# Kernel optimization log

Measured on AMD Instinct MI355X. Metric: run time of the kernel, lower is better.

The kernel has to match this reference:

```python
import jax, jax.numpy as jnp
import numpy as np

B, C_IN, C_OUT, N, E = 1, 64, 64, 100000, 3200000
BN_EPS = 1e-5


def setup_inputs() -> dict:
    key = jax.random.key(0)
    ks = jax.random.split(key, 8)
    return {
        "in_features": jax.random.normal(ks[0], (B, C_IN, N), dtype=jnp.float32),
        "w_v": jax.random.normal(ks[1], (C_OUT, C_IN), dtype=jnp.float32) * (1.0 / np.sqrt(C_IN)),
        "w_n": jax.random.normal(ks[2], (C_OUT, C_IN), dtype=jnp.float32) * (1.0 / np.sqrt(C_IN)),
        "gamma": jnp.ones((C_OUT,), dtype=jnp.float32),
        "beta": jnp.zeros((C_OUT,), dtype=jnp.float32),
        "prelu_a": jnp.full((1,), 0.25, dtype=jnp.float32),
        "reduce_index": jax.random.randint(ks[3], (E,), 0, N, dtype=jnp.int32),
        "gather_index": jax.random.randint(ks[4], (E,), 0, N, dtype=jnp.int32),
    }


def reference(in_features, w_v, w_n, gamma, beta, prelu_a, reduce_index, gather_index):
    # 1x1 convs == per-node linear maps: [B, C_in, N] -> [B, C_out, N]
    F_v = jnp.einsum('oi,bin->bon', w_v, in_features)
    F_n = jnp.einsum('oi,bin->bon', w_n, in_features)

    # gather source-node features per edge: [E, B, C_out]
    src = jnp.moveaxis(F_n[:, :, gather_index], 2, 0)
    # scatter-mean into destination nodes (include_self=False -> 0 for isolated nodes)
    sums = jax.ops.segment_sum(src, reduce_index, num_segments=N)  # [N, B, C]
    counts = jax.ops.segment_sum(jnp.ones((src.shape[0],), src.dtype), reduce_index,
                                 num_segments=N)  # [N]
    mean = sums / jnp.maximum(counts, 1.0)[:, None, None]  # nodes w/o edges stay 0
    out = jnp.moveaxis(mean, 0, 2) + F_v  # [B, C, N]

    # BatchNorm1d (training mode: biased batch stats over (B, N))
    mu = jnp.mean(out, axis=(0, 2), keepdims=True)
    var = jnp.mean((out - mu) ** 2, axis=(0, 2), keepdims=True)
    out = (out - mu) * jax.lax.rsqrt(var + BN_EPS)
    out = out * gamma[None, :, None] + beta[None, :, None]

    # PReLU with a single shared learnable slope
    out = jnp.where(out >= 0, out, prelu_a[0] * out)
    return out
```

## Files before the change

kernel.cpp:

```cpp
#include <hip/hip_runtime.h>
#include <hip/hip_bf16.h>

#define NODES 100000
#define BN_EPS 1e-5f
#define NB2 256
#define NPB2 391
#define CAP 13072
#define EPB 2048

__device__ __forceinline__ unsigned bf16rne(float f) {
    unsigned u = __float_as_uint(f);
    u += 0x7FFFu + ((u >> 16) & 1u);
    return u >> 16;
}
__device__ __forceinline__ float bflo(unsigned u) { return __uint_as_float(u << 16); }
__device__ __forceinline__ float bfhi(unsigned u) { return __uint_as_float(u & 0xFFFF0000u); }

__global__ __launch_bounds__(256, 8) void k_place(
        const int* __restrict__ ridx, const int* __restrict__ gidx,
        int* __restrict__ cursor, unsigned* __restrict__ packed, int E) {
    __shared__ int lh[4][NB2];
    const int t = threadIdx.x;
    const int w = t >> 6;
    for (int k = t; k < 4 * NB2; k += 256) ((int*)lh)[k] = 0;
    __syncthreads();
    const int base = blockIdx.x * EPB;
    int r[EPB / 256], g[EPB / 256];
#pragma unroll
    for (int k = 0; k < EPB / 256; ++k) {
        int e = base + t + (k << 8);
        r[k] = (e < E) ? ridx[e] : -1;
        g[k] = (e < E) ? gidx[e] : 0;
    }
#pragma unroll
    for (int k = 0; k < EPB / 256; ++k)
        if (r[k] >= 0) atomicAdd(&lh[w][(unsigned)r[k] / NPB2], 1);
    __syncthreads();
    {
        int c0 = lh[0][t], c1 = lh[1][t], c2 = lh[2][t], c3 = lh[3][t];
        int tot = c0 + c1 + c2 + c3;
        if (tot) {
            int g0 = t * CAP + atomicAdd(&cursor[t], tot);
            lh[0][t] = g0;
            lh[1][t] = g0 + c0;
            lh[2][t] = g0 + c0 + c1;
            lh[3][t] = g0 + c0 + c1 + c2;
        }
    }
    __syncthreads();
#pragma unroll
    for (int k = 0; k < EPB / 256; ++k) {
        if (r[k] >= 0) {
            unsigned rr = (unsigned)r[k];
            unsigned b = rr / NPB2;
            int off = atomicAdd(&lh[w][b], 1);
            if (off < (int)((b + 1) * CAP))
                packed[off] = ((rr - b * NPB2) << 17) | (unsigned)g[k];
        }
    }
}

__global__ __launch_bounds__(1024) void k_sortb(
        const int* __restrict__ cursor, unsigned* __restrict__ packed,
        int* __restrict__ nodestart, int* __restrict__ cnt) {
    __shared__ int lh[1024];
    __shared__ int lsc[1024];
    const int b = blockIdx.x, t = threadIdx.x;
    const int s0b = b * CAP;
    int cntb = cursor[b];
    if (cntb > CAP) cntb = CAP;
    unsigned r[(CAP + 1023) / 1024];
#pragma unroll
    for (int kk = 0; kk < (CAP + 1023) / 1024; ++kk) {
        int k = t + kk * 1024;
        if (k < cntb) r[kk] = packed[s0b + k];
    }
    lh[t] = 0;
    __syncthreads();
#pragma unroll
    for (int kk = 0; kk < (CAP + 1023) / 1024; ++kk) {
        int k = t + kk * 1024;
        if (k < cntb) atomicAdd(&lh[r[kk] >> 17], 1);
    }
    __syncthreads();
    lsc[t] = lh[t];
    __syncthreads();
    for (int off = 1; off < 1024; off <<= 1) {
        int v = lsc[t];
        int add = (t >= off) ? lsc[t - off] : 0;
        __syncthreads();
        lsc[t] = v + add;
        __syncthreads();
    }
    int excl = (t == 0) ? 0 : lsc[t - 1];
    if (t < NPB2) {
        int n = b * NPB2 + t;
        if (n < NODES) {
            nodestart[n] = s0b + excl;
            cnt[n] = lh[t];
        }
    }
    __syncthreads();
    lh[t] = excl;
    __syncthreads();
#pragma unroll
    for (int kk = 0; kk < (CAP + 1023) / 1024; ++kk) {
        int k = t + kk * 1024;
        if (k < cntb) {
            unsigned v = r[kk];
            int pos = atomicAdd(&lh[v >> 17], 1);
            packed[s0b + pos] = v & 0x1FFFFu;
        }
    }
}

__global__ __launch_bounds__(256, 4) void k_gemm_bf16(
        const float* __restrict__ x, const float* __restrict__ wn,
        unsigned* __restrict__ Fnh2) {
    __shared__ float lx[64 * 68];
    __shared__ float wt[64 * 68];
    const int t = threadIdx.x;
    const int n0 = blockIdx.x * 64;
    for (int idx = t; idx < 1024; idx += 256) {
        int rr = idx >> 4;
        int q4 = (idx & 15) * 4;
        int n = n0 + q4;
        float4 xv = {0.f, 0.f, 0.f, 0.f};
        if (n < NODES) xv = *(const float4*)(x + rr * NODES + n);
        *(float4*)&lx[rr * 68 + q4] = xv;
        float4 w4 = *(const float4*)(wn + (idx << 2));
        wt[(q4 + 0) * 68 + rr] = w4.x;
        wt[(q4 + 1) * 68 + rr] = w4.y;
        wt[(q4 + 2) * 68 + rr] = w4.z;
        wt[(q4 + 3) * 68 + rr] = w4.w;
    }
    __syncthreads();
    const int c4 = (t & 15) * 4;
    const int j4 = (t >> 4) * 4;
    float4 a0 = {0,0,0,0}, a1 = {0,0,0,0}, a2 = {0,0,0,0}, a3 = {0,0,0,0};
#pragma unroll 8
    for (int ci = 0; ci < 64; ++ci) {
        float4 w = *(const float4*)&wt[ci * 68 + c4];
        float4 xv = *(const float4*)&lx[ci * 68 + j4];
        a0.x += w.x * xv.x; a0.y += w.x * xv.y; a0.z += w.x * xv.z; a0.w += w.x * xv.w;
        a1.x += w.y * xv.x; a1.y += w.y * xv.y; a1.z += w.y * xv.z; a1.w += w.y * xv.w;
        a2.x += w.z * xv.x; a2.y += w.z * xv.y; a2.z += w.z * xv.z; a2.w += w.z * xv.w;
        a3.x += w.w * xv.x; a3.y += w.w * xv.y; a3.z += w.w * xv.z; a3.w += w.w * xv.w;
    }
    uint2* F2 = (uint2*)Fnh2;
#pragma unroll
    for (int k = 0; k < 4; ++k) {
        int n = n0 + j4 + k;
        if (n < NODES) {
            float v0 = (k == 0) ? a0.x : (k == 1) ? a0.y : (k == 2) ? a0.z : a0.w;
            float v1 = (k == 0) ? a1.x : (k == 1) ? a1.y : (k == 2) ? a1.z : a1.w;
            float v2 = (k == 0) ? a2.x : (k == 1) ? a2.y : (k == 2) ? a2.z : a2.w;
            float v3 = (k == 0) ? a3.x : (k == 1) ? a3.y : (k == 2) ? a3.z : a3.w;
            uint2 val;
            val.x = bf16rne(v0) | (bf16rne(v1) << 16);
            val.y = bf16rne(v2) | (bf16rne(v3) << 16);
            F2[n * 16 + (c4 >> 2)] = val;
        }
    }
}

__global__ __launch_bounds__(256) void k_gemm_n(
        const float* __restrict__ x, const float* __restrict__ wn,
        float* __restrict__ Fn) {
    __shared__ float lx[64][65];
    __shared__ float lw[64][65];
    const int t = threadIdx.x;
    const int n0 = blockIdx.x * 64;
    for (int idx = t; idx < 4096; idx += 256) {
        int r = idx >> 6, q = idx & 63;
        lw[r][q] = wn[idx];
        int n = n0 + q;
        lx[r][q] = (n < NODES) ? x[r * NODES + n] : 0.f;
    }
    __syncthreads();
    const int c = t & 63;
    const int jb = t >> 6;
    for (int k = 0; k < 16; ++k) {
        int j = jb + 4 * k;
        int n = n0 + j;
        if (n >= NODES) continue;
        float acc = 0.f;
#pragma unroll
        for (int ci = 0; ci < 64; ++ci)
            acc += lw[c][ci] * lx[ci][j];
        Fn[n * 64 + c] = acc;
    }
}

__global__ __launch_bounds__(256) void k_segreduce(
        const unsigned* __restrict__ Fnh2, const unsigned* __restrict__ packed,
        const int* __restrict__ nodestart, const int* __restrict__ cnt,
        float4* __restrict__ mean4) {
    const int n = (int)((blockIdx.x * 256u + threadIdx.x) >> 6);
    if (n >= NODES) return;
    const int lane = threadIdx.x & 63;
    const int sub = lane >> 3;
    const int cp  = lane & 7;
    const int s0 = nodestart[n];
    const int cn = cnt[n];
    const int s1 = s0 + cn;
    float f0 = 0.f, f1 = 0.f, f2 = 0.f, f3 = 0.f;
    float f4 = 0.f, f5 = 0.f, f6 = 0.f, f7 = 0.f;
    int i = s0;
    for (; i + 15 < s1; i += 16) {
        int ga = (int)packed[i + sub];
        int gb = (int)packed[i + 8 + sub];
        uint4 ua = *(const uint4*)(Fnh2 + (((size_t)ga) << 5) + (cp << 2));
        uint4 ub = *(const uint4*)(Fnh2 + (((size_t)gb) << 5) + (cp << 2));
        f0 += bflo(ua.x) + bflo(ub.x);
        f1 += bfhi(ua.x) + bfhi(ub.x);
        f2 += bflo(ua.y) + bflo(ub.y);
        f3 += bfhi(ua.y) + bfhi(ub.y);
        f4 += bflo(ua.z) + bflo(ub.z);
        f5 += bfhi(ua.z) + bfhi(ub.z);
        f6 += bflo(ua.w) + bflo(ub.w);
        f7 += bfhi(ua.w) + bfhi(ub.w);
    }
    for (; i < s1; i += 8) {
        uint4 u = {0u, 0u, 0u, 0u};
        if (i + sub < s1) {
            int g = (int)packed[i + sub];
            u = *(const uint4*)(Fnh2 + (((size_t)g) << 5) + (cp << 2));
        }
        f0 += bflo(u.x); f1 += bfhi(u.x);
        f2 += bflo(u.y); f3 += bfhi(u.y);
        f4 += bflo(u.z); f5 += bfhi(u.z);
        f6 += bflo(u.w); f7 += bfhi(u.w);
    }
#pragma unroll
    for (int m = 8; m < 64; m <<= 1) {
        f0 += __shfl_xor(f0, m);
        f1 += __shfl_xor(f1, m);
        f2 += __shfl_xor(f2, m);
        f3 += __shfl_xor(f3, m);
        f4 += __shfl_xor(f4, m);
        f5 += __shfl_xor(f5, m);
        f6 += __shfl_xor(f6, m);
        f7 += __shfl_xor(f7, m);
    }
    if (sub == 0) {
        float inv = 1.f / fmaxf((float)cn, 1.f);
        float4 lo4, hi4;
        lo4.x = f0 * inv; lo4.y = f1 * inv; lo4.z = f2 * inv; lo4.w = f3 * inv;
        hi4.x = f4 * inv; hi4.y = f5 * inv; hi4.z = f6 * inv; hi4.w = f7 * inv;
        mean4[n * 16 + cp * 2]     = lo4;
        mean4[n * 16 + cp * 2 + 1] = hi4;
    }
}

__global__ __launch_bounds__(256, 4) void k_combine(
        const float* __restrict__ x, const float* __restrict__ wv,
        const float* __restrict__ sums, const int* __restrict__ counts,
        const int divide,
        float* __restrict__ outpre, float* __restrict__ bn) {
    __shared__ float lx[64 * 68];
    __shared__ float wt[64 * 68];
    __shared__ float reds[64][5];
    __shared__ float redq[64][5];
    const int t = threadIdx.x;
    const int n0 = blockIdx.x * 64;
    const int c4 = (t & 15) * 4;
    const int j4 = (t >> 4) * 4;
    float4 mv[4];
    const float4* sums4 = (const float4*)sums;
#pragma unroll
    for (int k = 0; k < 4; ++k) {
        int n = n0 + j4 + k;
        mv[k] = (n < NODES) ? sums4[n * 16 + (c4 >> 2)]
                            : float4{0.f, 0.f, 0.f, 0.f};
    }
    for (int idx = t; idx < 1024; idx += 256) {
        int rr = idx >> 4;
        int q4 = (idx & 15) * 4;
        int n = n0 + q4;
        float4 xv = {0.f, 0.f, 0.f, 0.f};
        if (n < NODES) xv = *(const float4*)(x + rr * NODES + n);
        *(float4*)&lx[rr * 68 + q4] = xv;
        float4 w4 = *(const float4*)(wv + (idx << 2));
        wt[(q4 + 0) * 68 + rr] = w4.x;
        wt[(q4 + 1) * 68 + rr] = w4.y;
        wt[(q4 + 2) * 68 + rr] = w4.z;
        wt[(q4 + 3) * 68 + rr] = w4.w;
    }
    __syncthreads();
    float4 a0 = {0,0,0,0}, a1 = {0,0,0,0}, a2 = {0,0,0,0}, a3 = {0,0,0,0};
#pragma unroll 8
    for (int ci = 0; ci < 64; ++ci) {
        float4 w = *(const float4*)&wt[ci * 68 + c4];
        float4 xv = *(const float4*)&lx[ci * 68 + j4];
        a0.x += w.x * xv.x; a0.y += w.x * xv.y; a0.z += w.x * xv.z; a0.w += w.x * xv.w;
        a1.x += w.y * xv.x; a1.y += w.y * xv.y; a1.z += w.y * xv.z; a1.w += w.y * xv.w;
        a2.x += w.z * xv.x; a2.y += w.z * xv.y; a2.z += w.z * xv.z; a2.w += w.z * xv.w;
        a3.x += w.w * xv.x; a3.y += w.w * xv.y; a3.z += w.w * xv.z; a3.w += w.w * xv.w;
    }
    __syncthreads();
    float* tile = wt;
    float ls0 = 0.f, ls1 = 0.f, ls2 = 0.f, ls3 = 0.f;
    float lq0 = 0.f, lq1 = 0.f, lq2 = 0.f, lq3 = 0.f;
#pragma unroll
    for (int k = 0; k < 4; ++k) {
        int j = j4 + k;
        int n = n0 + j;
        float v0 = 0.f, v1 = 0.f, v2 = 0.f, v3 = 0.f;
        if (n < NODES) {
            float4 m = mv[k];
            if (divide) {
                float cf = fmaxf((float)counts[n], 1.f);
                m.x /= cf; m.y /= cf; m.z /= cf; m.w /= cf;
            }
            float b0 = (k == 0) ? a0.x : (k == 1) ? a0.y : (k == 2) ? a0.z : a0.w;
            float b1 = (k == 0) ? a1.x : (k == 1) ? a1.y : (k == 2) ? a1.z : a1.w;
            float b2 = (k == 0) ? a2.x : (k == 1) ? a2.y : (k == 2) ? a2.z : a2.w;
            float b3 = (k == 0) ? a3.x : (k == 1) ? a3.y : (k == 2) ? a3.z : a3.w;
            v0 = m.x + b0; v1 = m.y + b1; v2 = m.z + b2; v3 = m.w + b3;
            ls0 += v0; lq0 += v0 * v0;
            ls1 += v1; lq1 += v1 * v1;
            ls2 += v2; lq2 += v2 * v2;
            ls3 += v3; lq3 += v3 * v3;
        }
        tile[(c4 + 0) * 65 + j] = v0;
        tile[(c4 + 1) * 65 + j] = v1;
        tile[(c4 + 2) * 65 + j] = v2;
        tile[(c4 + 3) * 65 + j] = v3;
    }
    const int lane = t & 63;
    const int wid = t >> 6;
#pragma unroll
    for (int m = 16; m < 64; m <<= 1) {
        ls0 += __shfl_xor(ls0, m); lq0 += __shfl_xor(lq0, m);
        ls1 += __shfl_xor(ls1, m); lq1 += __shfl_xor(lq1, m);
        ls2 += __shfl_xor(ls2, m); lq2 += __shfl_xor(lq2, m);
        ls3 += __shfl_xor(ls3, m); lq3 += __shfl_xor(lq3, m);
    }
    if (lane < 16) {
        reds[lane * 4 + 0][wid] = ls0; redq[lane * 4 + 0][wid] = lq0;
        reds[lane * 4 + 1][wid] = ls1; redq[lane * 4 + 1][wid] = lq1;
        reds[lane * 4 + 2][wid] = ls2; redq[lane * 4 + 2][wid] = lq2;
        reds[lane * 4 + 3][wid] = ls3; redq[lane * 4 + 3][wid] = lq3;
    }
    __syncthreads();
    const int j2 = t & 63;
    const int c2 = t >> 6;
    const int n = n0 + j2;
    if (n < NODES) {
        for (int k = 0; k < 16; ++k) {
            int cc = c2 + 4 * k;
            outpre[cc * NODES + n] = tile[cc * 65 + j2];
        }
    }
    if (t < 64) {
        float s = reds[t][0] + reds[t][1] + reds[t][2] + reds[t][3];
        float q = redq[t][0] + redq[t][1] + redq[t][2] + redq[t][3];
        atomicAdd(&bn[t], s);
        atomicAdd(&bn[64 + t], q);
    }
}

__global__ __launch_bounds__(256) void k_final(
        float* __restrict__ out, const float* __restrict__ bn,
        const float* __restrict__ gamma, const float* __restrict__ beta,
        const float* __restrict__ pa) {
    const int c = blockIdx.y;
    const int n = blockIdx.x * 256 + threadIdx.x;
    const float invN = 1.f / (float)NODES;
    float mu = bn[c] * invN;
    float var = fmaxf(bn[64 + c] * invN - mu * mu, 0.f);
    float scale = gamma[c] * rsqrtf(var + BN_EPS);
    float shift = beta[c] - mu * scale;
    float a = pa[0];
    if (n < NODES) {
        float y = out[c * NODES + n] * scale + shift;
        y = (y >= 0.f) ? y : a * y;
        out[c * NODES + n] = y;
    }
}

__global__ __launch_bounds__(256) void k_scatter(
        const float* __restrict__ Fn,
        const int* __restrict__ gidx, const int* __restrict__ ridx,
        float* __restrict__ sums, int* __restrict__ counts, int E) {
    const int wave = (int)((blockIdx.x * blockDim.x + threadIdx.x) >> 6);
    const int lane = threadIdx.x & 63;
    const int base = wave * 64;
    if (base >= E) return;
    const int nvalid = min(64, E - base);
    int g = 0, r = 0;
    if (lane < nvalid) {
        g = gidx[base + lane];
        r = ridx[base + lane];
        atomicAdd(&counts[r], 1);
    }
    for (int i = 0; i < nvalid; ++i) {
        int gg = __shfl(g, i);
        int rr = __shfl(r, i);
        float v = Fn[gg * 64 + lane];
        atomicAdd(&sums[rr * 64 + lane], v);
    }
}

extern "C" void kernel_launch(void* const* d_in, const int* in_sizes, int n_in,
                              void* d_out, int out_size, void* d_ws, size_t ws_size,
                              hipStream_t stream) {
    const float* x     = (const float*)d_in[0];
    const float* w_v   = (const float*)d_in[1];
    const float* w_n   = (const float*)d_in[2];
    const float* gamma = (const float*)d_in[3];
    const float* beta  = (const float*)d_in[4];
    const float* pa    = (const float*)d_in[5];
    const int* ridx    = (const int*)d_in[6];
    const int* gidx    = (const int*)d_in[7];
    float* out = (float*)d_out;

    const int E = in_sizes[6];
    const long long N64 = (long long)NODES * 64;
    const int ntiles = (NODES + 63) / 64;
    const dim3 g4((NODES + 255) / 256, 64);

    size_t need = ((size_t)N64 + (size_t)NB2 * CAP + NB2 + 128
                   + NODES + NODES) * 4;

    if (ws_size >= need) {
        float*    mean      = (float*)d_ws;
        unsigned* packed    = (unsigned*)(mean + N64);
        int*      cursor    = (int*)(packed + (size_t)NB2 * CAP);
        float*    bn        = (float*)(cursor + NB2);
        int*      nodestart = (int*)(bn + 128);
        int*      cntarr    = nodestart + NODES;
        unsigned* Fnh2 = (unsigned*)out;

        hipMemsetAsync(cursor, 0, (NB2 + 128) * sizeof(int), stream);
        k_place<<<(E + EPB - 1) / EPB, 256, 0, stream>>>(ridx, gidx, cursor,
                                                         packed, E);
        k_gemm_bf16<<<ntiles, 256, 0, stream>>>(x, w_n, Fnh2);
        k_sortb<<<NB2, 1024, 0, stream>>>(cursor, packed, nodestart, cntarr);
        k_segreduce<<<(NODES * 64 + 255) / 256, 256, 0, stream>>>(
            Fnh2, packed, nodestart, cntarr, (float4*)mean);
        k_combine<<<ntiles, 256, 0, stream>>>(x, w_v, mean, cntarr, 0, out, bn);
        k_final<<<g4, 256, 0, stream>>>(out, bn, gamma, beta, pa);
    } else {
        float* sums   = (float*)d_ws;
        int*   counts = (int*)(sums + N64);
        float* bn     = (float*)(sums + N64 + NODES);
        float* Fn = out;

        hipMemsetAsync(sums, 0, (size_t)(N64 + NODES + 128) * sizeof(float),
                       stream);
        k_gemm_n<<<ntiles, 256, 0, stream>>>(x, w_n, Fn);
        k_scatter<<<(E + 255) / 256, 256, 0, stream>>>(Fn, gidx, ridx, sums,
                                                       counts, E);
        k_combine<<<ntiles, 256, 0, stream>>>(x, w_v, sums, counts, 1, out, bn);
        k_final<<<g4, 256, 0, stream>>>(out, bn, gamma, beta, pa);
    }
}
```

Measured before the change: 293.6 us.

## Split bf16 gathered features into channel planes and reduce per plane

The GEMM now writes F_n in bf16 as four planes of 16 channels each (32 bytes per node per plane) instead of one interleaved 128-byte row. The segment reduce runs four times, once per plane, so each pass touches a 3.2 MB working set that fits better in cache for the random gathers. The edge index loads use nontemporal hints. In exchange, the packed indices and node starts are re-read four times and there are four launches instead of one.

```diff
diff --git a/kernel.cpp b/kernel.cpp
--- a/kernel.cpp
+++ b/kernel.cpp
@@ -148,6 +148,8 @@
         a3.x += w.w * xv.x; a3.y += w.w * xv.y; a3.z += w.w * xv.z; a3.w += w.w * xv.w;
     }
     uint2* F2 = (uint2*)Fnh2;
+    const int kb = c4 >> 4;
+    const int d2 = (c4 & 15) >> 2;
 #pragma unroll
     for (int k = 0; k < 4; ++k) {
         int n = n0 + j4 + k;
@@ -159,7 +161,7 @@
             uint2 val;
             val.x = bf16rne(v0) | (bf16rne(v1) << 16);
             val.y = bf16rne(v2) | (bf16rne(v3) << 16);
-            F2[n * 16 + (c4 >> 2)] = val;
+            F2[(size_t)kb * (NODES * 4) + n * 4 + d2] = val;
         }
     }
 }
@@ -192,64 +194,51 @@
     }
 }
 
-__global__ __launch_bounds__(256) void k_segreduce(
-        const unsigned* __restrict__ Fnh2, const unsigned* __restrict__ packed,
+__global__ __launch_bounds__(256) void k_segreduce_p(
+        const unsigned* __restrict__ plane, const unsigned* __restrict__ packed,
         const int* __restrict__ nodestart, const int* __restrict__ cnt,
-        float4* __restrict__ mean4) {
+        float4* __restrict__ mean4, const int kb4) {
     const int n = (int)((blockIdx.x * 256u + threadIdx.x) >> 6);
     if (n >= NODES) return;
     const int lane = threadIdx.x & 63;
-    const int sub = lane >> 3;
-    const int cp  = lane & 7;
+    const int sub = lane >> 2;
+    const int cp  = lane & 3;
     const int s0 = nodestart[n];
     const int cn = cnt[n];
     const int s1 = s0 + cn;
     float f0 = 0.f, f1 = 0.f, f2 = 0.f, f3 = 0.f;
-    float f4 = 0.f, f5 = 0.f, f6 = 0.f, f7 = 0.f;
     int i = s0;
-    for (; i + 15 < s1; i += 16) {
-        int ga = (int)packed[i + sub];
-        int gb = (int)packed[i + 8 + sub];
-        uint4 ua = *(const uint4*)(Fnh2 + (((size_t)ga) << 5) + (cp << 2));
-        uint4 ub = *(const uint4*)(Fnh2 + (((size_t)gb) << 5) + (cp << 2));
+    for (; i + 31 < s1; i += 32) {
+        int ga = (int)__builtin_nontemporal_load(&packed[i + sub]);
+        int gb = (int)__builtin_nontemporal_load(&packed[i + 16 + sub]);
+        uint2 ua = *(const uint2*)(plane + (((size_t)ga) << 3) + (cp << 1));
+        uint2 ub = *(const uint2*)(plane + (((size_t)gb) << 3) + (cp << 1));
         f0 += bflo(ua.x) + bflo(ub.x);
         f1 += bfhi(ua.x) + bfhi(ub.x);
         f2 += bflo(ua.y) + bflo(ub.y);
         f3 += bfhi(ua.y) + bfhi(ub.y);
-        f4 += bflo(ua.z) + bflo(ub.z);
-        f5 += bfhi(ua.z) + bfhi(ub.z);
-        f6 += bflo(ua.w) + bflo(ub.w);
-        f7 += bfhi(ua.w) + bfhi(ub.w);
-    }
-    for (; i < s1; i += 8) {
-        uint4 u = {0u, 0u, 0u, 0u};
+    }
+    for (; i < s1; i += 16) {
+        uint2 u = {0u, 0u};
         if (i + sub < s1) {
             int g = (int)packed[i + sub];
-            u = *(const uint4*)(Fnh2 + (((size_t)g) << 5) + (cp << 2));
+            u = *(const uint2*)(plane + (((size_t)g) << 3) + (cp << 1));
         }
         f0 += bflo(u.x); f1 += bfhi(u.x);
         f2 += bflo(u.y); f3 += bfhi(u.y);
-        f4 += bflo(u.z); f5 += bfhi(u.z);
-        f6 += bflo(u.w); f7 += bfhi(u.w);
-    }
-#pragma unroll
-    for (int m = 8; m < 64; m <<= 1) {
+    }
+#pragma unroll
+    for (int m = 4; m < 64; m <<= 1) {
         f0 += __shfl_xor(f0, m);
         f1 += __shfl_xor(f1, m);
         f2 += __shfl_xor(f2, m);
         f3 += __shfl_xor(f3, m);
-        f4 += __shfl_xor(f4, m);
-        f5 += __shfl_xor(f5, m);
-        f6 += __shfl_xor(f6, m);
-        f7 += __shfl_xor(f7, m);
     }
     if (sub == 0) {
         float inv = 1.f / fmaxf((float)cn, 1.f);
-        float4 lo4, hi4;
-        lo4.x = f0 * inv; lo4.y = f1 * inv; lo4.z = f2 * inv; lo4.w = f3 * inv;
-        hi4.x = f4 * inv; hi4.y = f5 * inv; hi4.z = f6 * inv; hi4.w = f7 * inv;
-        mean4[n * 16 + cp * 2]     = lo4;
-        mean4[n * 16 + cp * 2 + 1] = hi4;
+        float4 v;
+        v.x = f0 * inv; v.y = f1 * inv; v.z = f2 * inv; v.w = f3 * inv;
+        mean4[n * 16 + kb4 + cp] = v;
     }
 }
 
@@ -438,8 +427,11 @@
                                                          packed, E);
         k_gemm_bf16<<<ntiles, 256, 0, stream>>>(x, w_n, Fnh2);
         k_sortb<<<NB2, 1024, 0, stream>>>(cursor, packed, nodestart, cntarr);
-        k_segreduce<<<(NODES * 64 + 255) / 256, 256, 0, stream>>>(
-            Fnh2, packed, nodestart, cntarr, (float4*)mean);
+        for (int kb = 0; kb < 4; ++kb) {
+            k_segreduce_p<<<(NODES * 64 + 255) / 256, 256, 0, stream>>>(
+                Fnh2 + (size_t)kb * NODES * 8, packed, nodestart, cntarr,
+                (float4*)mean, kb * 4);
+        }
         k_combine<<<ntiles, 256, 0, stream>>>(x, w_v, mean, cntarr, 0, out, bn);
         k_final<<<g4, 256, 0, stream>>>(out, bn, gamma, beta, pa);
     } else {
```

After: 397.0 us. 1.35x slower.

## Stream x directly from global in combine and store float4 outputs without LDS tile

Applied to the files above, without the earlier changes.

The combine kernel no longer stages the input feature tile in shared memory. Each thread now reads float4 slices of x straight from global memory inside the channel loop, and writes its 4x4 output block as float4 stores directly to outpre instead of transposing through an LDS tile. This drops one LDS buffer and one barrier and raises the occupancy hint from 4 to 8 blocks. The trade-off is that x is re-read by the 16 channel-group threads per node group, relying on cache hits, and the output stores are 16-byte strided writes rather than coalesced row writes.

```diff
diff --git a/kernel.cpp b/kernel.cpp
--- a/kernel.cpp
+++ b/kernel.cpp
@@ -253,81 +253,78 @@
     }
 }
 
-__global__ __launch_bounds__(256, 4) void k_combine(
+__global__ __launch_bounds__(256, 8) void k_combine(
         const float* __restrict__ x, const float* __restrict__ wv,
         const float* __restrict__ sums, const int* __restrict__ counts,
         const int divide,
         float* __restrict__ outpre, float* __restrict__ bn) {
-    __shared__ float lx[64 * 68];
     __shared__ float wt[64 * 68];
     __shared__ float reds[64][5];
     __shared__ float redq[64][5];
     const int t = threadIdx.x;
     const int n0 = blockIdx.x * 64;
-    const int c4 = (t & 15) * 4;
-    const int j4 = (t >> 4) * 4;
-    float4 mv[4];
-    const float4* sums4 = (const float4*)sums;
-#pragma unroll
-    for (int k = 0; k < 4; ++k) {
-        int n = n0 + j4 + k;
-        mv[k] = (n < NODES) ? sums4[n * 16 + (c4 >> 2)]
-                            : float4{0.f, 0.f, 0.f, 0.f};
-    }
     for (int idx = t; idx < 1024; idx += 256) {
-        int rr = idx >> 4;
-        int q4 = (idx & 15) * 4;
-        int n = n0 + q4;
-        float4 xv = {0.f, 0.f, 0.f, 0.f};
-        if (n < NODES) xv = *(const float4*)(x + rr * NODES + n);
-        *(float4*)&lx[rr * 68 + q4] = xv;
-        float4 w4 = *(const float4*)(wv + (idx << 2));
+        int rr = idx & 63;
+        int q4 = (idx >> 6) * 4;
+        float4 w4 = *(const float4*)(wv + rr * 64 + q4);
         wt[(q4 + 0) * 68 + rr] = w4.x;
         wt[(q4 + 1) * 68 + rr] = w4.y;
         wt[(q4 + 2) * 68 + rr] = w4.z;
         wt[(q4 + 3) * 68 + rr] = w4.w;
     }
     __syncthreads();
+    const int c4 = (t & 15) * 4;
+    const int j4 = (t >> 4) * 4;
+    const int jn = n0 + j4;
+    const bool valid = (jn < NODES);
+    const int jc = valid ? jn : 0;
     float4 a0 = {0,0,0,0}, a1 = {0,0,0,0}, a2 = {0,0,0,0}, a3 = {0,0,0,0};
-#pragma unroll 8
+#pragma unroll 4
     for (int ci = 0; ci < 64; ++ci) {
         float4 w = *(const float4*)&wt[ci * 68 + c4];
-        float4 xv = *(const float4*)&lx[ci * 68 + j4];
+        float4 xv = *(const float4*)(x + (size_t)ci * NODES + jc);
         a0.x += w.x * xv.x; a0.y += w.x * xv.y; a0.z += w.x * xv.z; a0.w += w.x * xv.w;
         a1.x += w.y * xv.x; a1.y += w.y * xv.y; a1.z += w.y * xv.z; a1.w += w.y * xv.w;
         a2.x += w.z * xv.x; a2.y += w.z * xv.y; a2.z += w.z * xv.z; a2.w += w.z * xv.w;
         a3.x += w.w * xv.x; a3.y += w.w * xv.y; a3.z += w.w * xv.z; a3.w += w.w * xv.w;
     }
-    __syncthreads();
-    float* tile = wt;
-    float ls0 = 0.f, ls1 = 0.f, ls2 = 0.f, ls3 = 0.f;
-    float lq0 = 0.f, lq1 = 0.f, lq2 = 0.f, lq3 = 0.f;
-#pragma unroll
-    for (int k = 0; k < 4; ++k) {
-        int j = j4 + k;
-        int n = n0 + j;
-        float v0 = 0.f, v1 = 0.f, v2 = 0.f, v3 = 0.f;
-        if (n < NODES) {
-            float4 m = mv[k];
-            if (divide) {
-                float cf = fmaxf((float)counts[n], 1.f);
-                m.x /= cf; m.y /= cf; m.z /= cf; m.w /= cf;
-            }
-            float b0 = (k == 0) ? a0.x : (k == 1) ? a0.y : (k == 2) ? a0.z : a0.w;
-            float b1 = (k == 0) ? a1.x : (k == 1) ? a1.y : (k == 2) ? a1.z : a1.w;
-            float b2 = (k == 0) ? a2.x : (k == 1) ? a2.y : (k == 2) ? a2.z : a2.w;
-            float b3 = (k == 0) ? a3.x : (k == 1) ? a3.y : (k == 2) ? a3.z : a3.w;
-            v0 = m.x + b0; v1 = m.y + b1; v2 = m.z + b2; v3 = m.w + b3;
-            ls0 += v0; lq0 += v0 * v0;
-            ls1 += v1; lq1 += v1 * v1;
-            ls2 += v2; lq2 += v2 * v2;
-            ls3 += v3; lq3 += v3 * v3;
-        }
-        tile[(c4 + 0) * 65 + j] = v0;
-        tile[(c4 + 1) * 65 + j] = v1;
-        tile[(c4 + 2) * 65 + j] = v2;
-        tile[(c4 + 3) * 65 + j] = v3;
-    }
+    const float4* sums4 = (const float4*)sums;
+    float4 mv0 = {0,0,0,0}, mv1 = {0,0,0,0}, mv2 = {0,0,0,0}, mv3 = {0,0,0,0};
+    if (valid) {
+        mv0 = sums4[(jn + 0) * 16 + (c4 >> 2)];
+        mv1 = sums4[(jn + 1) * 16 + (c4 >> 2)];
+        mv2 = sums4[(jn + 2) * 16 + (c4 >> 2)];
+        mv3 = sums4[(jn + 3) * 16 + (c4 >> 2)];
+        if (divide) {
+            float i0 = 1.f / fmaxf((float)counts[jn + 0], 1.f);
+            float i1 = 1.f / fmaxf((float)counts[jn + 1], 1.f);
+            float i2 = 1.f / fmaxf((float)counts[jn + 2], 1.f);
+            float i3 = 1.f / fmaxf((float)counts[jn + 3], 1.f);
+            mv0.x *= i0; mv0.y *= i0; mv0.z *= i0; mv0.w *= i0;
+            mv1.x *= i1; mv1.y *= i1; mv1.z *= i1; mv1.w *= i1;
+            mv2.x *= i2; mv2.y *= i2; mv2.z *= i2; mv2.w *= i2;
+            mv3.x *= i3; mv3.y *= i3; mv3.z *= i3; mv3.w *= i3;
+        }
+    }
+    float4 st0 = {0,0,0,0}, st1 = {0,0,0,0}, st2 = {0,0,0,0}, st3 = {0,0,0,0};
+    if (valid) {
+        st0.x = mv0.x + a0.x; st0.y = mv1.x + a0.y; st0.z = mv2.x + a0.z; st0.w = mv3.x + a0.w;
+        st1.x = mv0.y + a1.x; st1.y = mv1.y + a1.y; st1.z = mv2.y + a1.z; st1.w = mv3.y + a1.w;
+        st2.x = mv0.z + a2.x; st2.y = mv1.z + a2.y; st2.z = mv2.z + a2.z; st2.w = mv3.z + a2.w;
+        st3.x = mv0.w + a3.x; st3.y = mv1.w + a3.y; st3.z = mv2.w + a3.z; st3.w = mv3.w + a3.w;
+        *(float4*)(outpre + (size_t)(c4 + 0) * NODES + jn) = st0;
+        *(float4*)(outpre + (size_t)(c4 + 1) * NODES + jn) = st1;
+        *(float4*)(outpre + (size_t)(c4 + 2) * NODES + jn) = st2;
+        *(float4*)(outpre + (size_t)(c4 + 3) * NODES + jn) = st3;
+    }
+    float ls0 = st0.x + st0.y + st0.z + st0.w;
+    float ls1 = st1.x + st1.y + st1.z + st1.w;
+    float ls2 = st2.x + st2.y + st2.z + st2.w;
+    float ls3 = st3.x + st3.y + st3.z + st3.w;
+    float lq0 = st0.x*st0.x + st0.y*st0.y + st0.z*st0.z + st0.w*st0.w;
+    float lq1 = st1.x*st1.x + st1.y*st1.y + st1.z*st1.z + st1.w*st1.w;
+    float lq2 = st2.x*st2.x + st2.y*st2.y + st2.z*st2.z + st2.w*st2.w;
+    float lq3 = st3.x*st3.x + st3.y*st3.y + st3.z*st3.z + st3.w*st3.w;
     const int lane = t & 63;
     const int wid = t >> 6;
 #pragma unroll
@@ -344,15 +341,6 @@
         reds[lane * 4 + 3][wid] = ls3; redq[lane * 4 + 3][wid] = lq3;
     }
     __syncthreads();
-    const int j2 = t & 63;
-    const int c2 = t >> 6;
-    const int n = n0 + j2;
-    if (n < NODES) {
-        for (int k = 0; k < 16; ++k) {
-            int cc = c2 + 4 * k;
-            outpre[cc * NODES + n] = tile[cc * 65 + j2];
-        }
-    }
     if (t < 64) {
         float s = reds[t][0] + reds[t][1] + reds[t][2] + reds[t][3];
         float q = redq[t][0] + redq[t][1] + redq[t][2] + redq[t][3];
```

Result: slower. 300.5 us (+2.4%).

## Aggregate raw inputs before applying neighbor weight matrix, fuse both GEMMs in combine

Applied to the files above, without the earlier changes.

Exploits linearity of the neighbor 1x1 conv: the edge mean is computed over bf16-transposed input features, and W_n is applied afterwards inside the combine kernel alongside W_v. The standalone neighbor GEMM kernel becomes a plain transpose/convert kernel. This removes a separate GEMM pass and its compute in exchange for an extra in-tile GEMM and transposed staging of the mean in the combine kernel; bf16 rounding now applies to inputs rather than projected features.

```diff
diff --git a/kernel.cpp b/kernel.cpp
--- a/kernel.cpp
+++ b/kernel.cpp
@@ -114,11 +114,9 @@
     }
 }
 
-__global__ __launch_bounds__(256, 4) void k_gemm_bf16(
-        const float* __restrict__ x, const float* __restrict__ wn,
-        unsigned* __restrict__ Fnh2) {
+__global__ __launch_bounds__(256, 4) void k_xpose(
+        const float* __restrict__ x, unsigned* __restrict__ xb2) {
     __shared__ float lx[64 * 68];
-    __shared__ float wt[64 * 68];
     const int t = threadIdx.x;
     const int n0 = blockIdx.x * 64;
     for (int idx = t; idx < 1024; idx += 256) {
@@ -126,36 +124,21 @@
         int q4 = (idx & 15) * 4;
         int n = n0 + q4;
         float4 xv = {0.f, 0.f, 0.f, 0.f};
-        if (n < NODES) xv = *(const float4*)(x + rr * NODES + n);
+        if (n < NODES) xv = *(const float4*)(x + (size_t)rr * NODES + n);
         *(float4*)&lx[rr * 68 + q4] = xv;
-        float4 w4 = *(const float4*)(wn + (idx << 2));
-        wt[(q4 + 0) * 68 + rr] = w4.x;
-        wt[(q4 + 1) * 68 + rr] = w4.y;
-        wt[(q4 + 2) * 68 + rr] = w4.z;
-        wt[(q4 + 3) * 68 + rr] = w4.w;
     }
     __syncthreads();
     const int c4 = (t & 15) * 4;
     const int j4 = (t >> 4) * 4;
-    float4 a0 = {0,0,0,0}, a1 = {0,0,0,0}, a2 = {0,0,0,0}, a3 = {0,0,0,0};
-#pragma unroll 8
-    for (int ci = 0; ci < 64; ++ci) {
-        float4 w = *(const float4*)&wt[ci * 68 + c4];
-        float4 xv = *(const float4*)&lx[ci * 68 + j4];
-        a0.x += w.x * xv.x; a0.y += w.x * xv.y; a0.z += w.x * xv.z; a0.w += w.x * xv.w;
-        a1.x += w.y * xv.x; a1.y += w.y * xv.y; a1.z += w.y * xv.z; a1.w += w.y * xv.w;
-        a2.x += w.z * xv.x; a2.y += w.z * xv.y; a2.z += w.z * xv.z; a2.w += w.z * xv.w;
-        a3.x += w.w * xv.x; a3.y += w.w * xv.y; a3.z += w.w * xv.z; a3.w += w.w * xv.w;
-    }
-    uint2* F2 = (uint2*)Fnh2;
+    uint2* F2 = (uint2*)xb2;
 #pragma unroll
     for (int k = 0; k < 4; ++k) {
         int n = n0 + j4 + k;
         if (n < NODES) {
-            float v0 = (k == 0) ? a0.x : (k == 1) ? a0.y : (k == 2) ? a0.z : a0.w;
-            float v1 = (k == 0) ? a1.x : (k == 1) ? a1.y : (k == 2) ? a1.z : a1.w;
-            float v2 = (k == 0) ? a2.x : (k == 1) ? a2.y : (k == 2) ? a2.z : a2.w;
-            float v3 = (k == 0) ? a3.x : (k == 1) ? a3.y : (k == 2) ? a3.z : a3.w;
+            float v0 = lx[(c4 + 0) * 68 + j4 + k];
+            float v1 = lx[(c4 + 1) * 68 + j4 + k];
+            float v2 = lx[(c4 + 2) * 68 + j4 + k];
+            float v3 = lx[(c4 + 3) * 68 + j4 + k];
             uint2 val;
             val.x = bf16rne(v0) | (bf16rne(v1) << 16);
             val.y = bf16rne(v2) | (bf16rne(v3) << 16);
@@ -253,7 +236,129 @@
     }
 }
 
-__global__ __launch_bounds__(256, 4) void k_combine(
+__global__ __launch_bounds__(256, 4) void k_combine128(
+        const float* __restrict__ x, const float* __restrict__ wv,
+        const float* __restrict__ wn, const float* __restrict__ meanx,
+        float* __restrict__ outpre, float* __restrict__ bn) {
+    __shared__ float lx[64 * 68];
+    __shared__ float wt[64 * 68];
+    __shared__ float reds[64][5];
+    __shared__ float redq[64][5];
+    const int t = threadIdx.x;
+    const int n0 = blockIdx.x * 64;
+    const int c4 = (t & 15) * 4;
+    const int j4 = (t >> 4) * 4;
+    for (int idx = t; idx < 1024; idx += 256) {
+        int rr = idx >> 4;
+        int q4 = (idx & 15) * 4;
+        int n = n0 + q4;
+        float4 xv = {0.f, 0.f, 0.f, 0.f};
+        if (n < NODES) xv = *(const float4*)(x + (size_t)rr * NODES + n);
+        *(float4*)&lx[rr * 68 + q4] = xv;
+        float4 w4 = *(const float4*)(wv + (idx << 2));
+        wt[(q4 + 0) * 68 + rr] = w4.x;
+        wt[(q4 + 1) * 68 + rr] = w4.y;
+        wt[(q4 + 2) * 68 + rr] = w4.z;
+        wt[(q4 + 3) * 68 + rr] = w4.w;
+    }
+    __syncthreads();
+    float4 a0 = {0,0,0,0}, a1 = {0,0,0,0}, a2 = {0,0,0,0}, a3 = {0,0,0,0};
+#pragma unroll 8
+    for (int ci = 0; ci < 64; ++ci) {
+        float4 w = *(const float4*)&wt[ci * 68 + c4];
+        float4 xv = *(const float4*)&lx[ci * 68 + j4];
+        a0.x += w.x * xv.x; a0.y += w.x * xv.y; a0.z += w.x * xv.z; a0.w += w.x * xv.w;
+        a1.x += w.y * xv.x; a1.y += w.y * xv.y; a1.z += w.y * xv.z; a1.w += w.y * xv.w;
+        a2.x += w.z * xv.x; a2.y += w.z * xv.y; a2.z += w.z * xv.z; a2.w += w.z * xv.w;
+        a3.x += w.w * xv.x; a3.y += w.w * xv.y; a3.z += w.w * xv.z; a3.w += w.w * xv.w;
+    }
+    __syncthreads();
+    for (int idx = t; idx < 1024; idx += 256) {
+        int j  = idx >> 4;
+        int ci4 = (idx & 15) * 4;
+        int n = n0 + j;
+        float4 m4 = {0.f, 0.f, 0.f, 0.f};
+        if (n < NODES) m4 = *(const float4*)(meanx + (size_t)n * 64 + ci4);
+        lx[(ci4 + 0) * 68 + j] = m4.x;
+        lx[(ci4 + 1) * 68 + j] = m4.y;
+        lx[(ci4 + 2) * 68 + j] = m4.z;
+        lx[(ci4 + 3) * 68 + j] = m4.w;
+        int rr = idx >> 4;
+        int q4 = (idx & 15) * 4;
+        float4 w4 = *(const float4*)(wn + (idx << 2));
+        wt[(q4 + 0) * 68 + rr] = w4.x;
+        wt[(q4 + 1) * 68 + rr] = w4.y;
+        wt[(q4 + 2) * 68 + rr] = w4.z;
+        wt[(q4 + 3) * 68 + rr] = w4.w;
+    }
+    __syncthreads();
+#pragma unroll 8
+    for (int ci = 0; ci < 64; ++ci) {
+        float4 w = *(const float4*)&wt[ci * 68 + c4];
+        float4 xv = *(const float4*)&lx[ci * 68 + j4];
+        a0.x += w.x * xv.x; a0.y += w.x * xv.y; a0.z += w.x * xv.z; a0.w += w.x * xv.w;
+        a1.x += w.y * xv.x; a1.y += w.y * xv.y; a1.z += w.y * xv.z; a1.w += w.y * xv.w;
+        a2.x += w.z * xv.x; a2.y += w.z * xv.y; a2.z += w.z * xv.z; a2.w += w.z * xv.w;
+        a3.x += w.w * xv.x; a3.y += w.w * xv.y; a3.z += w.w * xv.z; a3.w += w.w * xv.w;
+    }
+    __syncthreads();
+    float* tile = wt;
+    float ls0 = 0.f, ls1 = 0.f, ls2 = 0.f, ls3 = 0.f;
+    float lq0 = 0.f, lq1 = 0.f, lq2 = 0.f, lq3 = 0.f;
+#pragma unroll
+    for (int k = 0; k < 4; ++k) {
+        int j = j4 + k;
+        int n = n0 + j;
+        float v0 = 0.f, v1 = 0.f, v2 = 0.f, v3 = 0.f;
+        if (n < NODES) {
+            v0 = (k == 0) ? a0.x : (k == 1) ? a0.y : (k == 2) ? a0.z : a0.w;
+            v1 = (k == 0) ? a1.x : (k == 1) ? a1.y : (k == 2) ? a1.z : a1.w;
+            v2 = (k == 0) ? a2.x : (k == 1) ? a2.y : (k == 2) ? a2.z : a2.w;
+            v3 = (k == 0) ? a3.x : (k == 1) ? a3.y : (k == 2) ? a3.z : a3.w;
+            ls0 += v0; lq0 += v0 * v0;
+            ls1 += v1; lq1 += v1 * v1;
+            ls2 += v2; lq2 += v2 * v2;
+            ls3 += v3; lq3 += v3 * v3;
+        }
+        tile[(c4 + 0) * 65 + j] = v0;
+        tile[(c4 + 1) * 65 + j] = v1;
+        tile[(c4 + 2) * 65 + j] = v2;
+        tile[(c4 + 3) * 65 + j] = v3;
+    }
+    const int lane = t & 63;
+    const int wid = t >> 6;
+#pragma unroll
+    for (int m = 16; m < 64; m <<= 1) {
+        ls0 += __shfl_xor(ls0, m); lq0 += __shfl_xor(lq0, m);
+        ls1 += __shfl_xor(ls1, m); lq1 += __shfl_xor(lq1, m);
+        ls2 += __shfl_xor(ls2, m); lq2 += __shfl_xor(lq2, m);
+        ls3 += __shfl_xor(ls3, m); lq3 += __shfl_xor(lq3, m);
+    }
+    if (lane < 16) {
+        reds[lane * 4 + 0][wid] = ls0; redq[lane * 4 + 0][wid] = lq0;
+        reds[lane * 4 + 1][wid] = ls1; redq[lane * 4 + 1][wid] = lq1;
+        reds[lane * 4 + 2][wid] = ls2; redq[lane * 4 + 2][wid] = lq2;
+        reds[lane * 4 + 3][wid] = ls3; redq[lane * 4 + 3][wid] = lq3;
+    }
+    __syncthreads();
+    const int j2 = t & 63;
+    const int c2 = t >> 6;
+    const int n = n0 + j2;
+    if (n < NODES) {
+        for (int k = 0; k < 16; ++k) {
+            int cc = c2 + 4 * k;
+            outpre[cc * NODES + n] = tile[cc * 65 + j2];
+        }
+    }
+    if (t < 64) {
+        float s = reds[t][0] + reds[t][1] + reds[t][2] + reds[t][3];
+        float q = redq[t][0] + redq[t][1] + redq[t][2] + redq[t][3];
+        atomicAdd(&bn[t], s);
+        atomicAdd(&bn[64 + t], q);
+    }
+}
+
+__global__ __launch_bounds__(256, 4) void k_combine_fb(
         const float* __restrict__ x, const float* __restrict__ wv,
         const float* __restrict__ sums, const int* __restrict__ counts,
         const int divide,
@@ -279,7 +384,7 @@
         int q4 = (idx & 15) * 4;
         int n = n0 + q4;
         float4 xv = {0.f, 0.f, 0.f, 0.f};
-        if (n < NODES) xv = *(const float4*)(x + rr * NODES + n);
+        if (n < NODES) xv = *(const float4*)(x + (size_t)rr * NODES + n);
         *(float4*)&lx[rr * 68 + q4] = xv;
         float4 w4 = *(const float4*)(wv + (idx << 2));
         wt[(q4 + 0) * 68 + rr] = w4.x;
@@ -425,22 +530,22 @@
                    + NODES + NODES) * 4;
 
     if (ws_size >= need) {
-        float*    mean      = (float*)d_ws;
-        unsigned* packed    = (unsigned*)(mean + N64);
+        float*    meanx     = (float*)d_ws;
+        unsigned* packed    = (unsigned*)(meanx + N64);
         int*      cursor    = (int*)(packed + (size_t)NB2 * CAP);
         float*    bn        = (float*)(cursor + NB2);
         int*      nodestart = (int*)(bn + 128);
         int*      cntarr    = nodestart + NODES;
-        unsigned* Fnh2 = (unsigned*)out;
+        unsigned* xb = (unsigned*)out;
 
         hipMemsetAsync(cursor, 0, (NB2 + 128) * sizeof(int), stream);
         k_place<<<(E + EPB - 1) / EPB, 256, 0, stream>>>(ridx, gidx, cursor,
                                                          packed, E);
-        k_gemm_bf16<<<ntiles, 256, 0, stream>>>(x, w_n, Fnh2);
+        k_xpose<<<ntiles, 256, 0, stream>>>(x, xb);
         k_sortb<<<NB2, 1024, 0, stream>>>(cursor, packed, nodestart, cntarr);
         k_segreduce<<<(NODES * 64 + 255) / 256, 256, 0, stream>>>(
-            Fnh2, packed, nodestart, cntarr, (float4*)mean);
-        k_combine<<<ntiles, 256, 0, stream>>>(x, w_v, mean, cntarr, 0, out, bn);
+            xb, packed, nodestart, cntarr, (float4*)meanx);
+        k_combine128<<<ntiles, 256, 0, stream>>>(x, w_v, w_n, meanx, out, bn);
         k_final<<<g4, 256, 0, stream>>>(out, bn, gamma, beta, pa);
     } else {
         float* sums   = (float*)d_ws;
@@ -453,7 +558,7 @@
         k_gemm_n<<<ntiles, 256, 0, stream>>>(x, w_n, Fn);
         k_scatter<<<(E + 255) / 256, 256, 0, stream>>>(Fn, gidx, ridx, sums,
                                                        counts, E);
-        k_combine<<<ntiles, 256, 0, stream>>>(x, w_v, sums, counts, 1, out, bn);
+        k_combine_fb<<<ntiles, 256, 0, stream>>>(x, w_v, sums, counts, 1, out, bn);
         k_final<<<g4, 256, 0, stream>>>(out, bn, gamma, beta, pa);
     }
 }
```

After: 290.3 us. About the same (-1.1%).
